# Performance work log

Measured on AMD Instinct MI355X. Metric: run time of the kernel, lower is better.

## Reference

```python
import jax, jax.numpy as jnp
import numpy as np

N, E, F_IN, HID, HEADS, CLASSES = 50000, 800000, 128, 128, 4, 2
NEG_SLOPE = 0.2


def _gatv2_layer(x, Wl, Wr, att, bias, src, dst, heads, concat):
    # PyG GATv2Conv (share_weights=False, eval mode):
    #   e_ij = att . leaky_relu(Wl x_j + Wr x_i); alpha = segment_softmax over dst;
    #   out_i = sum_j alpha_ij * (Wl x_j)
    n = x.shape[0]
    c = att.shape[-1]
    xl = (x @ Wl).reshape(n, heads, c)   # source transform [N,H,C]
    xr = (x @ Wr).reshape(n, heads, c)   # target transform [N,H,C]
    e = jax.nn.leaky_relu(xl[src] + xr[dst], NEG_SLOPE)      # [E,H,C]
    logits = jnp.einsum('ehc,hc->eh', e, att)                # [E,H]
    m = jax.ops.segment_max(logits, dst, num_segments=n)     # stable softmax per dst
    p = jnp.exp(logits - m[dst])
    denom = jax.ops.segment_sum(p, dst, num_segments=n)
    alpha = p / (denom[dst] + 1e-16)                         # [E,H]
    out = jax.ops.segment_sum(alpha[:, :, None] * xl[src], dst, num_segments=n)  # [N,H,C]
    out = out.reshape(n, heads * c) if concat else out.mean(axis=1)
    return out + bias


def setup_inputs() -> dict:
    key = jax.random.key(0)
    ks = jax.random.split(key, 16)
    s = lambda fan_in: 1.0 / np.sqrt(fan_in)
    inp = {
        'x': jax.random.normal(ks[0], (N, F_IN), jnp.float32),
        'edge_idx': jax.random.randint(ks[1], (2, E), 0, N, jnp.int64),
        'w_in': jax.random.normal(ks[2], (F_IN, HID), jnp.float32) * s(F_IN),
        'b_in': jnp.zeros((HID,), jnp.float32),
        'wl1': jax.random.normal(ks[3], (HID, HEADS * HID), jnp.float32) * s(HID),
        'wr1': jax.random.normal(ks[4], (HID, HEADS * HID), jnp.float32) * s(HID),
        'att1': jax.random.normal(ks[5], (HEADS, HID), jnp.float32) * s(HID),
        'b1': jnp.zeros((HEADS * HID,), jnp.float32),
        'wl2': jax.random.normal(ks[6], (HEADS * HID, HID), jnp.float32) * s(HEADS * HID),
        'wr2': jax.random.normal(ks[7], (HEADS * HID, HID), jnp.float32) * s(HEADS * HID),
        'att2': jax.random.normal(ks[8], (1, HID), jnp.float32) * s(HID),
        'b2': jnp.zeros((HID,), jnp.float32),
        'w_out': jax.random.normal(ks[9], (HID, CLASSES), jnp.float32) * s(HID),
        'b_out': jnp.zeros((CLASSES,), jnp.float32),
    }
    return inp


def reference(x, edge_idx, w_in, b_in, wl1, wr1, att1, b1, wl2, wr2, att2, b2, w_out, b_out):
    n = x.shape[0]
    loops = jnp.arange(n, dtype=edge_idx.dtype)  # PyG add_self_loops=True
    src = jnp.concatenate([edge_idx[0], loops])
    dst = jnp.concatenate([edge_idx[1], loops])
    h = jax.nn.elu(x @ w_in + b_in)              # dropout is identity in eval
    h = jax.nn.elu(_gatv2_layer(h, wl1, wr1, att1, b1, src, dst, HEADS, True))
    h = jax.nn.elu(_gatv2_layer(h, wl2, wr2, att2, b2, src, dst, 1, False))
    logits = h @ w_out + b_out
    return jax.nn.log_softmax(logits, axis=1)
```

## Files before the change

### kernel.cpp

```cpp
#include <hip/hip_runtime.h>
#include <hip/hip_bf16.h>
#include <math.h>

#define F_IN   128
#define HID    128
#define HEADS  4
#define HC1    (HEADS*HID)
#define CLASSES 2
#define NEG_SLOPE 0.2f
#define LOG2E 1.44269504088896340736f

#define SCAN_CHUNK 2048

typedef __attribute__((ext_vector_type(8))) short short8;
typedef __attribute__((ext_vector_type(4))) float f32x4;

__global__ void zero_int_kernel(int* __restrict__ p, int n) {
    int i = blockIdx.x * blockDim.x + threadIdx.x;
    int stride = gridDim.x * blockDim.x;
    for (; i < n; i += stride) p[i] = 0;
}

__global__ void deg_kernel(const int* __restrict__ dst_arr, int* __restrict__ deg,
                           int E, int N) {
    int e = blockIdx.x * blockDim.x + threadIdx.x;
    if (e >= E) return;
    int d = dst_arr[e];
    if ((unsigned)d >= (unsigned)N) d = 0;
    atomicAdd(&deg[d], 1);
}

__global__ void scan_partial_kernel(const int* __restrict__ deg, int* __restrict__ bsum, int n) {
    __shared__ int sdata[256];
    int b = blockIdx.x, t = threadIdx.x;
    int base = b * SCAN_CHUNK;
    int s = 0;
    for (int i = t; i < SCAN_CHUNK; i += 256) {
        int idx = base + i;
        s += (idx < n) ? deg[idx] : 0;
    }
    sdata[t] = s;
    __syncthreads();
    for (int off = 128; off; off >>= 1) {
        if (t < off) sdata[t] += sdata[t + off];
        __syncthreads();
    }
    if (t == 0) bsum[b] = sdata[0];
}

__global__ void scan_bsums_kernel(int* __restrict__ bsum, int nb, int* __restrict__ row, int n) {
    if (blockIdx.x == 0 && threadIdx.x == 0) {
        int acc = 0;
        for (int i = 0; i < nb; ++i) { int v = bsum[i]; bsum[i] = acc; acc += v; }
        row[n] = acc;
    }
}

__global__ void scan_final_kernel(const int* __restrict__ deg, const int* __restrict__ bsum,
                                  int* __restrict__ row, int* __restrict__ cursor, int n) {
    __shared__ int tsum[256];
    int b = blockIdx.x, t = threadIdx.x;
    int base = b * SCAN_CHUNK + t * 8;
    int local[8];
    int s = 0;
    #pragma unroll
    for (int k = 0; k < 8; ++k) {
        int idx = base + k;
        int v = (idx < n) ? deg[idx] : 0;
        local[k] = s;
        s += v;
    }
    tsum[t] = s;
    __syncthreads();
    for (int off = 1; off < 256; off <<= 1) {
        int v = 0;
        if (t >= off) v = tsum[t - off];
        __syncthreads();
        if (t >= off) tsum[t] += v;
        __syncthreads();
    }
    int texcl = (t == 0) ? 0 : tsum[t - 1];
    int boff = bsum[b];
    #pragma unroll
    for (int k = 0; k < 8; ++k) {
        int idx = base + k;
        if (idx < n) {
            int v = boff + texcl + local[k];
            row[idx] = v;
            cursor[idx] = v;
        }
    }
}

__global__ void scatter_kernel(const int* __restrict__ src_arr, const int* __restrict__ dst_arr,
                               int* __restrict__ cursor, int* __restrict__ src_sorted,
                               int E, int N) {
    int e = blockIdx.x * blockDim.x + threadIdx.x;
    if (e >= E) return;
    int s = src_arr[e], d = dst_arr[e];
    if ((unsigned)s >= (unsigned)N) s = 0;
    if ((unsigned)d >= (unsigned)N) d = 0;
    int pos = atomicAdd(&cursor[d], 1);
    src_sorted[pos] = s;
}

__global__ void weights_prep_kernel(
    const float* __restrict__ w_in, const float* __restrict__ wl1,
    const float* __restrict__ wr1, const float* __restrict__ wl2,
    const float* __restrict__ wr2,
    __hip_bfloat16* __restrict__ w_inT, __hip_bfloat16* __restrict__ wT1l,
    __hip_bfloat16* __restrict__ wT1r, __hip_bfloat16* __restrict__ wT2l,
    __hip_bfloat16* __restrict__ wT2r)
{
    int t = blockIdx.x * blockDim.x + threadIdx.x;
    const int S0 = 128 * 128, S1 = 128 * 512;
    const float* w; __hip_bfloat16* wT; int K, Nn, idx;
    if (t < S0)                { w = w_in; wT = w_inT; K = 128; Nn = 128; idx = t; }
    else if (t < S0 + S1)      { w = wl1;  wT = wT1l;  K = 128; Nn = 512; idx = t - S0; }
    else if (t < S0 + 2 * S1)  { w = wr1;  wT = wT1r;  K = 128; Nn = 512; idx = t - S0 - S1; }
    else if (t < S0 + 3 * S1)  { w = wl2;  wT = wT2l;  K = 512; Nn = 128; idx = t - S0 - 2 * S1; }
    else if (t < S0 + 4 * S1)  { w = wr2;  wT = wT2r;  K = 512; Nn = 128; idx = t - S0 - 3 * S1; }
    else return;
    int n = idx / K, k = idx % K;
    wT[idx] = __float2bfloat16(w[(size_t)k * Nn + n]);
}

__global__ void f32_to_bf16_kernel(const float* __restrict__ in,
                                   __hip_bfloat16* __restrict__ outb, int n) {
    int i = blockIdx.x * blockDim.x + threadIdx.x;
    int stride = gridDim.x * blockDim.x;
    short* ob = (short*)outb;
    for (int base = i * 4; base < n; base += stride * 4) {
        float4 v = *(const float4*)(in + base);
        __hip_bfloat16 h0 = __float2bfloat16(v.x);
        __hip_bfloat16 h1 = __float2bfloat16(v.y);
        __hip_bfloat16 h2 = __float2bfloat16(v.z);
        __hip_bfloat16 h3 = __float2bfloat16(v.w);
        short4 sv;
        sv.x = *reinterpret_cast<short*>(&h0);
        sv.y = *reinterpret_cast<short*>(&h1);
        sv.z = *reinterpret_cast<short*>(&h2);
        sv.w = *reinterpret_cast<short*>(&h3);
        *(short4*)(ob + base) = sv;
    }
}

template<int ACT, typename OutT>
__global__ __launch_bounds__(256) void mfma_gemm_kernel(
    const __hip_bfloat16* __restrict__ A,
    const __hip_bfloat16* __restrict__ BT,
    const float* __restrict__ bias,
    OutT* __restrict__ C,
    int M, int K, int N)
{
    constexpr int BM = 128, BN = 128, BK = 64, LDA = 72;
    __shared__ __align__(16) short As[BM * LDA];
    __shared__ __align__(16) short Bs[BN * LDA];

    const int tid  = threadIdx.x;
    const int lane = tid & 63;
    const int wid  = tid >> 6;
    const int wm   = wid >> 1;
    const int wn   = wid & 1;
    const int fr   = lane & 15;
    const int fk   = (lane >> 4) * 8;

    const int row0 = blockIdx.y * BM;
    const int col0 = blockIdx.x * BN;

    const short* Ag = (const short*)A;
    const short* Bg = (const short*)BT;

    f32x4 acc[4][4] = {};

    for (int k0 = 0; k0 < K; k0 += BK) {
        #pragma unroll
        for (int it = 0; it < 4; ++it) {
            int chunk = it * 256 + tid;
            int r = chunk >> 3, c = chunk & 7;
            int gr = row0 + r;
            short8 v = {0, 0, 0, 0, 0, 0, 0, 0};
            if (gr < M) v = *(const short8*)(Ag + (size_t)gr * K + k0 + c * 8);
            *(short8*)(&As[r * LDA + c * 8]) = v;
        }
        #pragma unroll
        for (int it = 0; it < 4; ++it) {
            int chunk = it * 256 + tid;
            int n = chunk >> 3, c = chunk & 7;
            short8 v = *(const short8*)(Bg + (size_t)(col0 + n) * K + k0 + c * 8);
            *(short8*)(&Bs[n * LDA + c * 8]) = v;
        }
        __syncthreads();
        #pragma unroll
        for (int kk = 0; kk < 2; ++kk) {
            short8 af[4], bf[4];
            #pragma unroll
            for (int i = 0; i < 4; ++i)
                af[i] = *(const short8*)(&As[(wm * 64 + i * 16 + fr) * LDA + kk * 32 + fk]);
            #pragma unroll
            for (int j = 0; j < 4; ++j)
                bf[j] = *(const short8*)(&Bs[(wn * 64 + j * 16 + fr) * LDA + kk * 32 + fk]);
            #pragma unroll
            for (int i = 0; i < 4; ++i)
                #pragma unroll
                for (int j = 0; j < 4; ++j)
                    acc[i][j] = __builtin_amdgcn_mfma_f32_16x16x32_bf16(af[i], bf[j], acc[i][j], 0, 0, 0);
        }
        __syncthreads();
    }

    const int crow = row0 + wm * 64;
    const int ccol = col0 + wn * 64;
    #pragma unroll
    for (int i = 0; i < 4; ++i) {
        #pragma unroll
        for (int j = 0; j < 4; ++j) {
            int col = ccol + j * 16 + (lane & 15);
            float bv = bias ? bias[col] : 0.0f;
            #pragma unroll
            for (int reg = 0; reg < 4; ++reg) {
                int r = crow + i * 16 + (lane >> 4) * 4 + reg;
                if (r < M) {
                    float v = acc[i][j][reg] + bv;
                    if (ACT == 1) v = (v > 0.0f) ? v : expm1f(v);
                    C[(size_t)r * N + col] = (OutT)v;
                }
            }
        }
    }
}

__global__ __launch_bounds__(256) void gatv2_l1_fused_kernel(
    const __hip_bfloat16* __restrict__ xl, const __hip_bfloat16* __restrict__ xr,
    const int* __restrict__ row, const int* __restrict__ src_sorted,
    const float* __restrict__ att, const float* __restrict__ b1,
    __hip_bfloat16* __restrict__ out1, int N)
{
    int d = blockIdx.x * 4 + (threadIdx.x >> 6);
    if (d >= N) return;
    int lane = threadIdx.x & 63;
    int cbase = lane * 8;
    const short* xlb = (const short*)xl;

    float xrd[8], attv[8];
    {
        uint4 raw = *reinterpret_cast<const uint4*>((const short*)xr + (size_t)d * HC1 + cbase);
        const unsigned* u = reinterpret_cast<const unsigned*>(&raw);
        #pragma unroll
        for (int j = 0; j < 4; ++j) {
            xrd[2 * j]     = __uint_as_float(u[j] << 16);
            xrd[2 * j + 1] = __uint_as_float(u[j] & 0xffff0000u);
        }
        #pragma unroll
        for (int k = 0; k < 8; ++k) attv[k] = att[cbase + k] * LOG2E;
    }

    float m = -__builtin_huge_valf();
    float s = 0.0f;
    float o[8] = {};

    int rs = row[d], re = row[d + 1];

    uint4 raw = *reinterpret_cast<const uint4*>(xlb + (size_t)d * HC1 + cbase);
    for (int it = rs - 1; it < re; ++it) {
        uint4 cur = raw;
        if (it + 1 < re) {
            int sn = src_sorted[it + 1];
            raw = *reinterpret_cast<const uint4*>(xlb + (size_t)sn * HC1 + cbase);
        }
        float v[8];
        const unsigned* u = reinterpret_cast<const unsigned*>(&cur);
        #pragma unroll
        for (int j = 0; j < 4; ++j) {
            v[2 * j]     = __uint_as_float(u[j] << 16);
            v[2 * j + 1] = __uint_as_float(u[j] & 0xffff0000u);
        }
        float t = 0.0f;
        #pragma unroll
        for (int k = 0; k < 8; ++k) {
            float ek = v[k] + xrd[k];
            float e = fmaxf(ek, NEG_SLOPE * ek);
            t = fmaf(e, attv[k], t);
        }
        t += __shfl_xor(t, 1);
        t += __shfl_xor(t, 2);
        t += __shfl_xor(t, 4);
        t += __shfl_xor(t, 8);
        if (t > m) {
            float r = exp2f(m - t);
            s *= r;
            #pragma unroll
            for (int k = 0; k < 8; ++k) o[k] *= r;
            m = t;
        }
        float p = exp2f(t - m);
        s += p;
        #pragma unroll
        for (int k = 0; k < 8; ++k) o[k] = fmaf(p, v[k], o[k]);
    }

    float inv = 1.0f / (s + 1e-16f);
    short8 sv;
    #pragma unroll
    for (int k = 0; k < 8; ++k) {
        float val = o[k] * inv + b1[cbase + k];
        val = (val > 0.0f) ? val : expm1f(val);
        __hip_bfloat16 hb = __float2bfloat16(val);
        sv[k] = *reinterpret_cast<short*>(&hb);
    }
    *(short8*)((short*)out1 + (size_t)d * HC1 + cbase) = sv;
}

__global__ __launch_bounds__(256) void gatv2_l2_final_kernel(
    const __hip_bfloat16* __restrict__ xl2, const __hip_bfloat16* __restrict__ xr2,
    const int* __restrict__ row, const int* __restrict__ src_sorted,
    const float* __restrict__ att2, const float* __restrict__ b2,
    const float* __restrict__ w_out, const float* __restrict__ b_out,
    float* __restrict__ out, int N)
{
    int d = blockIdx.x * 4 + (threadIdx.x >> 6);
    if (d >= N) return;
    int lane = threadIdx.x & 63;
    int c0 = lane * 2;
    const short* xlb = (const short*)xl2;

    unsigned xr_raw = *reinterpret_cast<const unsigned*>((const short*)xr2 + (size_t)d * HID + c0);
    float xrd0 = __uint_as_float(xr_raw << 16);
    float xrd1 = __uint_as_float(xr_raw & 0xffff0000u);
    float a2x = att2[c0] * LOG2E;
    float a2y = att2[c0 + 1] * LOG2E;

    float m = -__builtin_huge_valf();
    float s = 0.0f;
    float o0 = 0.0f, o1 = 0.0f;

    int rs = row[d], re = row[d + 1];
    unsigned raw = *reinterpret_cast<const unsigned*>(xlb + (size_t)d * HID + c0);
    for (int it = rs - 1; it < re; ++it) {
        unsigned cur = raw;
        if (it + 1 < re) {
            int sn = src_sorted[it + 1];
            raw = *reinterpret_cast<const unsigned*>(xlb + (size_t)sn * HID + c0);
        }
        float v0 = __uint_as_float(cur << 16);
        float v1 = __uint_as_float(cur & 0xffff0000u);
        float e0 = v0 + xrd0; e0 = fmaxf(e0, NEG_SLOPE * e0);
        float e1 = v1 + xrd1; e1 = fmaxf(e1, NEG_SLOPE * e1);
        float t = fmaf(e0, a2x, e1 * a2y);
        #pragma unroll
        for (int off = 32; off; off >>= 1) t += __shfl_xor(t, off);
        if (t > m) {
            float r = exp2f(m - t);
            s *= r; o0 *= r; o1 *= r;
            m = t;
        }
        float p = exp2f(t - m);
        s += p;
        o0 = fmaf(p, v0, o0);
        o1 = fmaf(p, v1, o1);
    }

    float inv = 1.0f / (s + 1e-16f);
    float h0v = o0 * inv + b2[c0];
    float h1v = o1 * inv + b2[c0 + 1];
    h0v = (h0v > 0.0f) ? h0v : expm1f(h0v);
    h1v = (h1v > 0.0f) ? h1v : expm1f(h1v);

    float a0 = fmaf(h0v, w_out[c0 * 2 + 0], h1v * w_out[(c0 + 1) * 2 + 0]);
    float a1 = fmaf(h0v, w_out[c0 * 2 + 1], h1v * w_out[(c0 + 1) * 2 + 1]);
    #pragma unroll
    for (int off = 32; off; off >>= 1) {
        a0 += __shfl_xor(a0, off);
        a1 += __shfl_xor(a1, off);
    }
    if (lane == 0) {
        float z0 = a0 + b_out[0];
        float z1 = a1 + b_out[1];
        float mx = fmaxf(z0, z1);
        float lse = mx + logf(__expf(z0 - mx) + __expf(z1 - mx));
        out[(size_t)d * CLASSES + 0] = z0 - lse;
        out[(size_t)d * CLASSES + 1] = z1 - lse;
    }
}

extern "C" void kernel_launch(void* const* d_in, const int* in_sizes, int n_in,
                              void* d_out, int out_size, void* d_ws, size_t ws_size,
                              hipStream_t stream)
{
    const float* x     = (const float*)d_in[0];
    const int*   eidx  = (const int*)d_in[1];
    const float* w_in  = (const float*)d_in[2];
    const float* b_in  = (const float*)d_in[3];
    const float* wl1   = (const float*)d_in[4];
    const float* wr1   = (const float*)d_in[5];
    const float* att1  = (const float*)d_in[6];
    const float* b1    = (const float*)d_in[7];
    const float* wl2   = (const float*)d_in[8];
    const float* wr2   = (const float*)d_in[9];
    const float* att2  = (const float*)d_in[10];
    const float* b2    = (const float*)d_in[11];
    const float* w_out = (const float*)d_in[12];
    const float* b_out = (const float*)d_in[13];
    float* out = (float*)d_out;

    const int N = in_sizes[0] / F_IN;
    const int E = in_sizes[1] / 2;
    const int* src_arr = eidx;
    const int* dst_arr = eidx + E;

    size_t off = 0;
    auto alloc = [&](size_t bytes) -> char* {
        char* ptr = (char*)d_ws + off;
        off += (bytes + 255) & ~(size_t)255;
        return ptr;
    };
    int* row        = (int*)alloc((size_t)(N + 1) * 4);
    int* cursor     = (int*)alloc((size_t)N * 4);
    int* deg        = (int*)alloc((size_t)N * 4);
    int* bsum       = (int*)alloc(64 * 4);
    int* src_sorted = (int*)alloc((size_t)E * 4);
    __hip_bfloat16* w_inT = (__hip_bfloat16*)alloc((size_t)F_IN * HID * 2);
    __hip_bfloat16* wT1l  = (__hip_bfloat16*)alloc((size_t)HID * HC1 * 2);
    __hip_bfloat16* wT1r  = (__hip_bfloat16*)alloc((size_t)HID * HC1 * 2);
    __hip_bfloat16* wT2l  = (__hip_bfloat16*)alloc((size_t)HC1 * HID * 2);
    __hip_bfloat16* wT2r  = (__hip_bfloat16*)alloc((size_t)HC1 * HID * 2);
    __hip_bfloat16* xb    = (__hip_bfloat16*)alloc((size_t)N * F_IN * 2);
    __hip_bfloat16* h0b   = (__hip_bfloat16*)alloc((size_t)N * HID * 2);
    __hip_bfloat16* xl1   = (__hip_bfloat16*)alloc((size_t)N * HC1 * 2);
    __hip_bfloat16* xr1   = (__hip_bfloat16*)alloc((size_t)N * HC1 * 2);
    __hip_bfloat16* out1  = (__hip_bfloat16*)alloc((size_t)N * HC1 * 2);

    __hip_bfloat16* xl2 = xb;
    __hip_bfloat16* xr2 = h0b;

    dim3 blk(256);
    const int NB_SCAN = (N + SCAN_CHUNK - 1) / SCAN_CHUNK;

    hipLaunchKernelGGL(zero_int_kernel, dim3(64), blk, 0, stream, deg, N);
    hipLaunchKernelGGL(deg_kernel, dim3((E + 255) / 256), blk, 0, stream, dst_arr, deg, E, N);
    hipLaunchKernelGGL(scan_partial_kernel, dim3(NB_SCAN), blk, 0, stream, deg, bsum, N);
    hipLaunchKernelGGL(scan_bsums_kernel, dim3(1), blk, 0, stream, bsum, NB_SCAN, row, N);
    hipLaunchKernelGGL(scan_final_kernel, dim3(NB_SCAN), blk, 0, stream, deg, bsum, row, cursor, N);
    hipLaunchKernelGGL(scatter_kernel, dim3((E + 255) / 256), blk, 0, stream,
                       src_arr, dst_arr, cursor, src_sorted, E, N);

    {
        int total = 128 * 128 + 4 * 128 * 512;
        hipLaunchKernelGGL(weights_prep_kernel, dim3((total + 255) / 256), blk, 0, stream,
                           w_in, wl1, wr1, wl2, wr2, w_inT, wT1l, wT1r, wT2l, wT2r);
        hipLaunchKernelGGL(f32_to_bf16_kernel, dim3(2048), blk, 0, stream, x, xb, N * F_IN);
    }
    {
        dim3 grid(HID / 128, (N + 127) / 128);
        hipLaunchKernelGGL((mfma_gemm_kernel<1, __hip_bfloat16>), grid, blk, 0, stream,
                           xb, w_inT, b_in, h0b, N, F_IN, HID);
    }
    {
        dim3 grid(HC1 / 128, (N + 127) / 128);
        hipLaunchKernelGGL((mfma_gemm_kernel<0, __hip_bfloat16>), grid, blk, 0, stream,
                           h0b, wT1l, (const float*)nullptr, xl1, N, HID, HC1);
        hipLaunchKernelGGL((mfma_gemm_kernel<0, __hip_bfloat16>), grid, blk, 0, stream,
                           h0b, wT1r, (const float*)nullptr, xr1, N, HID, HC1);
    }
    {
        dim3 grid((N + 3) / 4);
        hipLaunchKernelGGL(gatv2_l1_fused_kernel, grid, blk, 0, stream,
                           xl1, xr1, row, src_sorted, att1, b1, out1, N);
    }
    {
        dim3 grid(HID / 128, (N + 127) / 128);
        hipLaunchKernelGGL((mfma_gemm_kernel<0, __hip_bfloat16>), grid, blk, 0, stream,
                           out1, wT2l, (const float*)nullptr, xl2, N, HC1, HID);
        hipLaunchKernelGGL((mfma_gemm_kernel<0, __hip_bfloat16>), grid, blk, 0, stream,
                           out1, wT2r, (const float*)nullptr, xr2, N, HC1, HID);
    }
    {
        dim3 grid((N + 3) / 4);
        hipLaunchKernelGGL(gatv2_l2_final_kernel, grid, blk, 0, stream,
                           xl2, xr2, row, src_sorted, att2, b2, w_out, b_out, out, N);
    }
}
```

Before: 588.4 us.

## Merge left/right GEMMs, fuse input bf16 cast, restructure layer-2 aggregation

The weight prep concatenates Wl and Wr so each GATv2 layer runs one GEMM producing an interleaved [N, 2*HC] xl|xr buffer instead of two launches. The standalone f32-to-bf16 conversion of x is dropped; the first GEMM now reads fp32 and converts while loading the tile. The layer-1 edge kernel uses packed float2 math, and the layer-2 kernel has four 16-lane groups process different edges in parallel, then merges their online-softmax states with shuffles. The interleaved layout doubles the row stride for gathers, and the layer-2 path adds a merge step in exchange for more edge parallelism.

```diff
diff --git a/kernel.cpp b/kernel.cpp
--- a/kernel.cpp
+++ b/kernel.cpp
@@ -9,11 +9,20 @@
 #define CLASSES 2
 #define NEG_SLOPE 0.2f
 #define LOG2E 1.44269504088896340736f
+#define MNEG  -3.0e38f
 
 #define SCAN_CHUNK 2048
 
 typedef __attribute__((ext_vector_type(8))) short short8;
 typedef __attribute__((ext_vector_type(4))) float f32x4;
+typedef __attribute__((ext_vector_type(2))) float f32x2;
+
+__device__ __forceinline__ f32x2 unpack2(unsigned u) {
+    f32x2 r;
+    r.x = __uint_as_float(u << 16);
+    r.y = __uint_as_float(u & 0xffff0000u);
+    return r;
+}
 
 __global__ void zero_int_kernel(int* __restrict__ p, int n) {
     int i = blockIdx.x * blockDim.x + threadIdx.x;
@@ -108,46 +117,36 @@
     const float* __restrict__ w_in, const float* __restrict__ wl1,
     const float* __restrict__ wr1, const float* __restrict__ wl2,
     const float* __restrict__ wr2,
-    __hip_bfloat16* __restrict__ w_inT, __hip_bfloat16* __restrict__ wT1l,
-    __hip_bfloat16* __restrict__ wT1r, __hip_bfloat16* __restrict__ wT2l,
-    __hip_bfloat16* __restrict__ wT2r)
+    __hip_bfloat16* __restrict__ w_inT, __hip_bfloat16* __restrict__ wT1,
+    __hip_bfloat16* __restrict__ wT2)
 {
     int t = blockIdx.x * blockDim.x + threadIdx.x;
     const int S0 = 128 * 128, S1 = 128 * 512;
-    const float* w; __hip_bfloat16* wT; int K, Nn, idx;
-    if (t < S0)                { w = w_in; wT = w_inT; K = 128; Nn = 128; idx = t; }
-    else if (t < S0 + S1)      { w = wl1;  wT = wT1l;  K = 128; Nn = 512; idx = t - S0; }
-    else if (t < S0 + 2 * S1)  { w = wr1;  wT = wT1r;  K = 128; Nn = 512; idx = t - S0 - S1; }
-    else if (t < S0 + 3 * S1)  { w = wl2;  wT = wT2l;  K = 512; Nn = 128; idx = t - S0 - 2 * S1; }
-    else if (t < S0 + 4 * S1)  { w = wr2;  wT = wT2r;  K = 512; Nn = 128; idx = t - S0 - 3 * S1; }
-    else return;
-    int n = idx / K, k = idx % K;
-    wT[idx] = __float2bfloat16(w[(size_t)k * Nn + n]);
-}
-
-__global__ void f32_to_bf16_kernel(const float* __restrict__ in,
-                                   __hip_bfloat16* __restrict__ outb, int n) {
-    int i = blockIdx.x * blockDim.x + threadIdx.x;
-    int stride = gridDim.x * blockDim.x;
-    short* ob = (short*)outb;
-    for (int base = i * 4; base < n; base += stride * 4) {
-        float4 v = *(const float4*)(in + base);
-        __hip_bfloat16 h0 = __float2bfloat16(v.x);
-        __hip_bfloat16 h1 = __float2bfloat16(v.y);
-        __hip_bfloat16 h2 = __float2bfloat16(v.z);
-        __hip_bfloat16 h3 = __float2bfloat16(v.w);
-        short4 sv;
-        sv.x = *reinterpret_cast<short*>(&h0);
-        sv.y = *reinterpret_cast<short*>(&h1);
-        sv.z = *reinterpret_cast<short*>(&h2);
-        sv.w = *reinterpret_cast<short*>(&h3);
-        *(short4*)(ob + base) = sv;
-    }
-}
-
-template<int ACT, typename OutT>
+    if (t < S0) {
+        int n = t / 128, k = t % 128;
+        w_inT[t] = __float2bfloat16(w_in[(size_t)k * 128 + n]);
+    } else if (t < S0 + S1) {
+        int idx = t - S0;
+        int n = idx / 128, k = idx % 128;
+        wT1[idx] = __float2bfloat16(wl1[(size_t)k * 512 + n]);
+    } else if (t < S0 + 2 * S1) {
+        int idx = t - S0 - S1;
+        int n = idx / 128, k = idx % 128;
+        wT1[(size_t)(512 + n) * 128 + k] = __float2bfloat16(wr1[(size_t)k * 512 + n]);
+    } else if (t < S0 + 3 * S1) {
+        int idx = t - S0 - 2 * S1;
+        int n = idx / 512, k = idx % 512;
+        wT2[idx] = __float2bfloat16(wl2[(size_t)k * 128 + n]);
+    } else if (t < S0 + 4 * S1) {
+        int idx = t - S0 - 3 * S1;
+        int n = idx / 512, k = idx % 512;
+        wT2[(size_t)(128 + n) * 512 + k] = __float2bfloat16(wr2[(size_t)k * 128 + n]);
+    }
+}
+
+template<int ACT, typename AT, typename OutT>
 __global__ __launch_bounds__(256) void mfma_gemm_kernel(
-    const __hip_bfloat16* __restrict__ A,
+    const AT* __restrict__ A,
     const __hip_bfloat16* __restrict__ BT,
     const float* __restrict__ bias,
     OutT* __restrict__ C,
@@ -168,7 +167,6 @@
     const int row0 = blockIdx.y * BM;
     const int col0 = blockIdx.x * BN;
 
-    const short* Ag = (const short*)A;
     const short* Bg = (const short*)BT;
 
     f32x4 acc[4][4] = {};
@@ -180,7 +178,24 @@
             int r = chunk >> 3, c = chunk & 7;
             int gr = row0 + r;
             short8 v = {0, 0, 0, 0, 0, 0, 0, 0};
-            if (gr < M) v = *(const short8*)(Ag + (size_t)gr * K + k0 + c * 8);
+            if (gr < M) {
+                if constexpr (sizeof(AT) == 2) {
+                    v = *(const short8*)((const short*)A + (size_t)gr * K + k0 + c * 8);
+                } else {
+                    const float* ap = (const float*)A + (size_t)gr * K + k0 + c * 8;
+                    float4 a0 = *(const float4*)ap;
+                    float4 a1 = *(const float4*)(ap + 4);
+                    __hip_bfloat16 h;
+                    h = __float2bfloat16(a0.x); v[0] = *(short*)&h;
+                    h = __float2bfloat16(a0.y); v[1] = *(short*)&h;
+                    h = __float2bfloat16(a0.z); v[2] = *(short*)&h;
+                    h = __float2bfloat16(a0.w); v[3] = *(short*)&h;
+                    h = __float2bfloat16(a1.x); v[4] = *(short*)&h;
+                    h = __float2bfloat16(a1.y); v[5] = *(short*)&h;
+                    h = __float2bfloat16(a1.z); v[6] = *(short*)&h;
+                    h = __float2bfloat16(a1.w); v[7] = *(short*)&h;
+                }
+            }
             *(short8*)(&As[r * LDA + c * 8]) = v;
         }
         #pragma unroll
@@ -231,7 +246,7 @@
 }
 
 __global__ __launch_bounds__(256) void gatv2_l1_fused_kernel(
-    const __hip_bfloat16* __restrict__ xl, const __hip_bfloat16* __restrict__ xr,
+    const __hip_bfloat16* __restrict__ xlr,
     const int* __restrict__ row, const int* __restrict__ src_sorted,
     const float* __restrict__ att, const float* __restrict__ b1,
     __hip_bfloat16* __restrict__ out1, int N)
@@ -240,48 +255,49 @@
     if (d >= N) return;
     int lane = threadIdx.x & 63;
     int cbase = lane * 8;
-    const short* xlb = (const short*)xl;
-
-    float xrd[8], attv[8];
-    {
-        uint4 raw = *reinterpret_cast<const uint4*>((const short*)xr + (size_t)d * HC1 + cbase);
+    const short* basep = (const short*)xlr;
+
+    f32x2 xrd2[4], attv2[4];
+    {
+        uint4 raw = *reinterpret_cast<const uint4*>(basep + (size_t)d * 1024 + 512 + cbase);
         const unsigned* u = reinterpret_cast<const unsigned*>(&raw);
         #pragma unroll
+        for (int j = 0; j < 4; ++j) xrd2[j] = unpack2(u[j]);
+        #pragma unroll
         for (int j = 0; j < 4; ++j) {
-            xrd[2 * j]     = __uint_as_float(u[j] << 16);
-            xrd[2 * j + 1] = __uint_as_float(u[j] & 0xffff0000u);
-        }
-        #pragma unroll
-        for (int k = 0; k < 8; ++k) attv[k] = att[cbase + k] * LOG2E;
-    }
-
-    float m = -__builtin_huge_valf();
+            attv2[j].x = att[cbase + 2 * j] * LOG2E;
+            attv2[j].y = att[cbase + 2 * j + 1] * LOG2E;
+        }
+    }
+
+    float m = MNEG;
     float s = 0.0f;
-    float o[8] = {};
+    f32x2 o2[4] = {};
 
     int rs = row[d], re = row[d + 1];
 
-    uint4 raw = *reinterpret_cast<const uint4*>(xlb + (size_t)d * HC1 + cbase);
+    uint4 raw = *reinterpret_cast<const uint4*>(basep + (size_t)d * 1024 + cbase);
     for (int it = rs - 1; it < re; ++it) {
         uint4 cur = raw;
         if (it + 1 < re) {
             int sn = src_sorted[it + 1];
-            raw = *reinterpret_cast<const uint4*>(xlb + (size_t)sn * HC1 + cbase);
-        }
-        float v[8];
+            raw = *reinterpret_cast<const uint4*>(basep + (size_t)sn * 1024 + cbase);
+        }
         const unsigned* u = reinterpret_cast<const unsigned*>(&cur);
+        f32x2 v2[4];
+        #pragma unroll
+        for (int j = 0; j < 4; ++j) v2[j] = unpack2(u[j]);
+
+        f32x2 tacc = {0.0f, 0.0f};
         #pragma unroll
         for (int j = 0; j < 4; ++j) {
-            v[2 * j]     = __uint_as_float(u[j] << 16);
-            v[2 * j + 1] = __uint_as_float(u[j] & 0xffff0000u);
-        }
-        float t = 0.0f;
-        #pragma unroll
-        for (int k = 0; k < 8; ++k) {
-            float ek = v[k] + xrd[k];
-            float e = fmaxf(ek, NEG_SLOPE * ek);
-            t = fmaf(e, attv[k], t);
-        }
+            f32x2 e = v2[j] + xrd2[j];
+            f32x2 ne = e * NEG_SLOPE;
+            e.x = fmaxf(e.x, ne.x);
+            e.y = fmaxf(e.y, ne.y);
+            tacc = __builtin_elementwise_fma(e, attv2[j], tacc);
+        }
+        float t = tacc.x + tacc.y;
         t += __shfl_xor(t, 1);
         t += __shfl_xor(t, 2);
         t += __shfl_xor(t, 4);
@@ -289,30 +305,35 @@
         if (t > m) {
             float r = exp2f(m - t);
             s *= r;
+            f32x2 r2 = {r, r};
             #pragma unroll
-            for (int k = 0; k < 8; ++k) o[k] *= r;
+            for (int j = 0; j < 4; ++j) o2[j] *= r2;
             m = t;
         }
         float p = exp2f(t - m);
         s += p;
-        #pragma unroll
-        for (int k = 0; k < 8; ++k) o[k] = fmaf(p, v[k], o[k]);
+        f32x2 p2 = {p, p};
+        #pragma unroll
+        for (int j = 0; j < 4; ++j) o2[j] = __builtin_elementwise_fma(p2, v2[j], o2[j]);
     }
 
     float inv = 1.0f / (s + 1e-16f);
     short8 sv;
     #pragma unroll
-    for (int k = 0; k < 8; ++k) {
-        float val = o[k] * inv + b1[cbase + k];
-        val = (val > 0.0f) ? val : expm1f(val);
-        __hip_bfloat16 hb = __float2bfloat16(val);
-        sv[k] = *reinterpret_cast<short*>(&hb);
+    for (int j = 0; j < 4; ++j) {
+        #pragma unroll
+        for (int h = 0; h < 2; ++h) {
+            float val = ((h == 0) ? o2[j].x : o2[j].y) * inv + b1[cbase + 2 * j + h];
+            val = (val > 0.0f) ? val : expm1f(val);
+            __hip_bfloat16 hb = __float2bfloat16(val);
+            sv[2 * j + h] = *reinterpret_cast<short*>(&hb);
+        }
     }
     *(short8*)((short*)out1 + (size_t)d * HC1 + cbase) = sv;
 }
 
 __global__ __launch_bounds__(256) void gatv2_l2_final_kernel(
-    const __hip_bfloat16* __restrict__ xl2, const __hip_bfloat16* __restrict__ xr2,
+    const __hip_bfloat16* __restrict__ xlr2,
     const int* __restrict__ row, const int* __restrict__ src_sorted,
     const float* __restrict__ att2, const float* __restrict__ b2,
     const float* __restrict__ w_out, const float* __restrict__ b_out,
@@ -321,55 +342,104 @@
     int d = blockIdx.x * 4 + (threadIdx.x >> 6);
     if (d >= N) return;
     int lane = threadIdx.x & 63;
-    int c0 = lane * 2;
-    const short* xlb = (const short*)xl2;
-
-    unsigned xr_raw = *reinterpret_cast<const unsigned*>((const short*)xr2 + (size_t)d * HID + c0);
-    float xrd0 = __uint_as_float(xr_raw << 16);
-    float xrd1 = __uint_as_float(xr_raw & 0xffff0000u);
-    float a2x = att2[c0] * LOG2E;
-    float a2y = att2[c0 + 1] * LOG2E;
-
-    float m = -__builtin_huge_valf();
+    int g  = lane >> 4;
+    int gl = lane & 15;
+    int cbase = gl * 8;
+    const short* basep = (const short*)xlr2;
+
+    f32x2 xrd2[4], attv2[4];
+    {
+        uint4 rawx = *reinterpret_cast<const uint4*>(basep + (size_t)d * 256 + 128 + cbase);
+        const unsigned* u = reinterpret_cast<const unsigned*>(&rawx);
+        #pragma unroll
+        for (int j = 0; j < 4; ++j) xrd2[j] = unpack2(u[j]);
+        #pragma unroll
+        for (int j = 0; j < 4; ++j) {
+            attv2[j].x = att2[cbase + 2 * j] * LOG2E;
+            attv2[j].y = att2[cbase + 2 * j + 1] * LOG2E;
+        }
+    }
+
+    float m = MNEG;
     float s = 0.0f;
-    float o0 = 0.0f, o1 = 0.0f;
+    f32x2 o2[4] = {};
 
     int rs = row[d], re = row[d + 1];
-    unsigned raw = *reinterpret_cast<const unsigned*>(xlb + (size_t)d * HID + c0);
-    for (int it = rs - 1; it < re; ++it) {
-        unsigned cur = raw;
-        if (it + 1 < re) {
-            int sn = src_sorted[it + 1];
-            raw = *reinterpret_cast<const unsigned*>(xlb + (size_t)sn * HID + c0);
-        }
-        float v0 = __uint_as_float(cur << 16);
-        float v1 = __uint_as_float(cur & 0xffff0000u);
-        float e0 = v0 + xrd0; e0 = fmaxf(e0, NEG_SLOPE * e0);
-        float e1 = v1 + xrd1; e1 = fmaxf(e1, NEG_SLOPE * e1);
-        float t = fmaf(e0, a2x, e1 * a2y);
-        #pragma unroll
-        for (int off = 32; off; off >>= 1) t += __shfl_xor(t, off);
+    int L = re - rs + 1;
+
+    for (int p0 = g; p0 < L; p0 += 4) {
+        int srcn = (p0 == 0) ? d : src_sorted[rs + p0 - 1];
+        uint4 cur = *reinterpret_cast<const uint4*>(basep + (size_t)srcn * 256 + cbase);
+        const unsigned* u = reinterpret_cast<const unsigned*>(&cur);
+        f32x2 v2[4];
+        #pragma unroll
+        for (int j = 0; j < 4; ++j) v2[j] = unpack2(u[j]);
+
+        f32x2 tacc = {0.0f, 0.0f};
+        #pragma unroll
+        for (int j = 0; j < 4; ++j) {
+            f32x2 e = v2[j] + xrd2[j];
+            f32x2 ne = e * NEG_SLOPE;
+            e.x = fmaxf(e.x, ne.x);
+            e.y = fmaxf(e.y, ne.y);
+            tacc = __builtin_elementwise_fma(e, attv2[j], tacc);
+        }
+        float t = tacc.x + tacc.y;
+        t += __shfl_xor(t, 1);
+        t += __shfl_xor(t, 2);
+        t += __shfl_xor(t, 4);
+        t += __shfl_xor(t, 8);
         if (t > m) {
             float r = exp2f(m - t);
-            s *= r; o0 *= r; o1 *= r;
+            s *= r;
+            f32x2 r2 = {r, r};
+            #pragma unroll
+            for (int j = 0; j < 4; ++j) o2[j] *= r2;
             m = t;
         }
         float p = exp2f(t - m);
         s += p;
-        o0 = fmaf(p, v0, o0);
-        o1 = fmaf(p, v1, o1);
+        f32x2 p2 = {p, p};
+        #pragma unroll
+        for (int j = 0; j < 4; ++j) o2[j] = __builtin_elementwise_fma(p2, v2[j], o2[j]);
+    }
+
+    #pragma unroll
+    for (int off = 16; off <= 32; off <<= 1) {
+        float m_o = __shfl_xor(m, off);
+        float s_o = __shfl_xor(s, off);
+        f32x2 oo[4];
+        #pragma unroll
+        for (int j = 0; j < 4; ++j) {
+            oo[j].x = __shfl_xor(o2[j].x, off);
+            oo[j].y = __shfl_xor(o2[j].y, off);
+        }
+        float mn = fmaxf(m, m_o);
+        float a = exp2f(m - mn);
+        float b = exp2f(m_o - mn);
+        s = s * a + s_o * b;
+        f32x2 a2 = {a, a}, b2v = {b, b};
+        #pragma unroll
+        for (int j = 0; j < 4; ++j)
+            o2[j] = o2[j] * a2 + oo[j] * b2v;
+        m = mn;
     }
 
     float inv = 1.0f / (s + 1e-16f);
-    float h0v = o0 * inv + b2[c0];
-    float h1v = o1 * inv + b2[c0 + 1];
-    h0v = (h0v > 0.0f) ? h0v : expm1f(h0v);
-    h1v = (h1v > 0.0f) ? h1v : expm1f(h1v);
-
-    float a0 = fmaf(h0v, w_out[c0 * 2 + 0], h1v * w_out[(c0 + 1) * 2 + 0]);
-    float a1 = fmaf(h0v, w_out[c0 * 2 + 1], h1v * w_out[(c0 + 1) * 2 + 1]);
-    #pragma unroll
-    for (int off = 32; off; off >>= 1) {
+    float a0 = 0.0f, a1 = 0.0f;
+    #pragma unroll
+    for (int j = 0; j < 4; ++j) {
+        #pragma unroll
+        for (int h = 0; h < 2; ++h) {
+            int c = cbase + 2 * j + h;
+            float val = ((h == 0) ? o2[j].x : o2[j].y) * inv + b2[c];
+            val = (val > 0.0f) ? val : expm1f(val);
+            a0 = fmaf(val, w_out[c * 2 + 0], a0);
+            a1 = fmaf(val, w_out[c * 2 + 1], a1);
+        }
+    }
+    #pragma unroll
+    for (int off = 1; off <= 8; off <<= 1) {
         a0 += __shfl_xor(a0, off);
         a1 += __shfl_xor(a1, off);
     }
@@ -420,18 +490,13 @@
     int* bsum       = (int*)alloc(64 * 4);
     int* src_sorted = (int*)alloc((size_t)E * 4);
     __hip_bfloat16* w_inT = (__hip_bfloat16*)alloc((size_t)F_IN * HID * 2);
-    __hip_bfloat16* wT1l  = (__hip_bfloat16*)alloc((size_t)HID * HC1 * 2);
-    __hip_bfloat16* wT1r  = (__hip_bfloat16*)alloc((size_t)HID * HC1 * 2);
-    __hip_bfloat16* wT2l  = (__hip_bfloat16*)alloc((size_t)HC1 * HID * 2);
-    __hip_bfloat16* wT2r  = (__hip_bfloat16*)alloc((size_t)HC1 * HID * 2);
-    __hip_bfloat16* xb    = (__hip_bfloat16*)alloc((size_t)N * F_IN * 2);
+    __hip_bfloat16* wT1   = (__hip_bfloat16*)alloc((size_t)2 * HC1 * HID * 2);
+    __hip_bfloat16* wT2   = (__hip_bfloat16*)alloc((size_t)2 * HID * HC1 * 2);
     __hip_bfloat16* h0b   = (__hip_bfloat16*)alloc((size_t)N * HID * 2);
-    __hip_bfloat16* xl1   = (__hip_bfloat16*)alloc((size_t)N * HC1 * 2);
-    __hip_bfloat16* xr1   = (__hip_bfloat16*)alloc((size_t)N * HC1 * 2);
+    __hip_bfloat16* xlr1  = (__hip_bfloat16*)alloc((size_t)N * 2 * HC1 * 2);
     __hip_bfloat16* out1  = (__hip_bfloat16*)alloc((size_t)N * HC1 * 2);
 
-    __hip_bfloat16* xl2 = xb;
-    __hip_bfloat16* xr2 = h0b;
+    __hip_bfloat16* xlr2 = xlr1;
 
     dim3 blk(256);
     const int NB_SCAN = (N + SCAN_CHUNK - 1) / SCAN_CHUNK;
@@ -447,36 +512,31 @@
     {
         int total = 128 * 128 + 4 * 128 * 512;
         hipLaunchKernelGGL(weights_prep_kernel, dim3((total + 255) / 256), blk, 0, stream,
-                           w_in, wl1, wr1, wl2, wr2, w_inT, wT1l, wT1r, wT2l, wT2r);
-        hipLaunchKernelGGL(f32_to_bf16_kernel, dim3(2048), blk, 0, stream, x, xb, N * F_IN);
+                           w_in, wl1, wr1, wl2, wr2, w_inT, wT1, wT2);
     }
     {
         dim3 grid(HID / 128, (N + 127) / 128);
-        hipLaunchKernelGGL((mfma_gemm_kernel<1, __hip_bfloat16>), grid, blk, 0, stream,
-                           xb, w_inT, b_in, h0b, N, F_IN, HID);
-    }
-    {
-        dim3 grid(HC1 / 128, (N + 127) / 128);
-        hipLaunchKernelGGL((mfma_gemm_kernel<0, __hip_bfloat16>), grid, blk, 0, stream,
-                           h0b, wT1l, (const float*)nullptr, xl1, N, HID, HC1);
-        hipLaunchKernelGGL((mfma_gemm_kernel<0, __hip_bfloat16>), grid, blk, 0, stream,
-                           h0b, wT1r, (const float*)nullptr, xr1, N, HID, HC1);
+        hipLaunchKernelGGL((mfma_gemm_kernel<1, float, __hip_bfloat16>), grid, blk, 0, stream,
+                           x, w_inT, b_in, h0b, N, F_IN, HID);
+    }
+    {
+        dim3 grid(2 * HC1 / 128, (N + 127) / 128);
+        hipLaunchKernelGGL((mfma_gemm_kernel<0, __hip_bfloat16, __hip_bfloat16>), grid, blk, 0, stream,
+                           h0b, wT1, (const float*)nullptr, xlr1, N, HID, 2 * HC1);
     }
     {
         dim3 grid((N + 3) / 4);
         hipLaunchKernelGGL(gatv2_l1_fused_kernel, grid, blk, 0, stream,
-                           xl1, xr1, row, src_sorted, att1, b1, out1, N);
-    }
-    {
-        dim3 grid(HID / 128, (N + 127) / 128);
-        hipLaunchKernelGGL((mfma_gemm_kernel<0, __hip_bfloat16>), grid, blk, 0, stream,
-                           out1, wT2l, (const float*)nullptr, xl2, N, HC1, HID);
-        hipLaunchKernelGGL((mfma_gemm_kernel<0, __hip_bfloat16>), grid, blk, 0, stream,
-                           out1, wT2r, (const float*)nullptr, xr2, N, HC1, HID);
+                           xlr1, row, src_sorted, att1, b1, out1, N);
+    }
+    {
+        dim3 grid(2 * HID / 128, (N + 127) / 128);
+        hipLaunchKernelGGL((mfma_gemm_kernel<0, __hip_bfloat16, __hip_bfloat16>), grid, blk, 0, stream,
+                           out1, wT2, (const float*)nullptr, xlr2, N, HC1, 2 * HID);
     }
     {
         dim3 grid((N + 3) / 4);
         hipLaunchKernelGGL(gatv2_l2_final_kernel, grid, blk, 0, stream,
-                           xl2, xr2, row, src_sorted, att2, b2, w_out, b_out, out, N);
-    }
-}
+                           xlr2, row, src_sorted, att2, b2, w_out, b_out, out, N);
+    }
+}
```

New measurement: 578.5 us. About the same (-1.7%).
